# Performance work log

Measured on AMD Instinct MI355X. Metric: run time of the kernel, lower is better.

## Reference

```python
import jax, jax.numpy as jnp
import numpy as np

H, W = 224, 224
WS = 7            # window size
SHIFT = 3         # shift_size = window_size // 2
C = 256           # embed_dim
NH = 4            # num heads
HD = C // NH      # head dim
N = WS * WS       # tokens per window
B = 4
HIDDEN = 1024
EPS = 1e-12


def _rel_pos_index():
    coords = np.stack(np.meshgrid(np.arange(WS), np.arange(WS), indexing='ij'))  # (2,WS,WS)
    cf = coords.reshape(2, -1)
    rel = (cf[:, :, None] - cf[:, None, :]).transpose(1, 2, 0)  # (N,N,2)
    rel[:, :, 0] += WS - 1
    rel[:, :, 1] += WS - 1
    rel[:, :, 0] *= 2 * WS - 1
    return rel.sum(-1)  # (N,N) int

REL_IDX = _rel_pos_index()


def _shift_mask():
    img = np.zeros((H, W))
    cnt = 0
    for hs in (slice(0, -WS), slice(-WS, -SHIFT), slice(-SHIFT, None)):
        for ws_ in (slice(0, -WS), slice(-WS, -SHIFT), slice(-SHIFT, None)):
            img[hs, ws_] = cnt
            cnt += 1
    mw = img.reshape(H // WS, WS, W // WS, WS).transpose(0, 2, 1, 3).reshape(-1, N)
    am = mw[:, None, :] - mw[:, :, None]  # (nW, N, N)
    return np.where(am != 0, -100.0, 0.0).astype(np.float32)

SHIFT_MASK = _shift_mask()  # (nW, N, N)


def layer_norm(x, g, b):
    mu = x.mean(-1, keepdims=True)
    var = ((x - mu) ** 2).mean(-1, keepdims=True)
    return (x - mu) / jnp.sqrt(var + EPS) * g + b


def partition(x, shift):
    x = x.reshape(B, H, W, C)
    if shift > 0:
        x = jnp.roll(x, (-shift, -shift), axis=(1, 2))
    x = x.reshape(B, H // WS, WS, W // WS, WS, C).transpose(0, 1, 3, 2, 4, 5)
    return x.reshape(-1, N, C)  # (B*nW, N, C)


def reverse(x, shift):
    x = x.reshape(B, H // WS, W // WS, WS, WS, C).transpose(0, 1, 3, 2, 4, 5).reshape(B, H, W, C)
    if shift > 0:
        x = jnp.roll(x, (shift, shift), axis=(1, 2))
    return x.reshape(B, H * W, C)


def window_attn(q, k, v, wq, bq, wk, bk, wv, bv, wp, bp, rpb, bool_mask, shift_mask):
    B_ = q.shape[0]
    scale = HD ** -0.5
    qh = (q @ wq + bq).reshape(B_, N, NH, HD).transpose(0, 2, 1, 3) * scale
    kh = (k @ wk + bk).reshape(B_, N, NH, HD).transpose(0, 2, 1, 3)
    vh = (v @ wv + bv).reshape(B_, N, NH, HD).transpose(0, 2, 1, 3)
    attn = jnp.einsum('bhnd,bhmd->bhnm', qh, kh)  # (B_, NH, N, N)
    attn = jnp.where(bool_mask, -1e9, attn)       # masked_fill_(attn_mask, -1e9)
    bias = rpb[REL_IDX.reshape(-1)].reshape(N, N, NH).transpose(2, 0, 1)  # (NH,N,N)
    attn = attn + bias[None]
    if shift_mask is not None:
        nW = shift_mask.shape[0]
        attn = attn.reshape(B_ // nW, nW, NH, N, N) + shift_mask[None, :, None]
        attn = attn.reshape(B_, NH, N, N)
    attn = jax.nn.softmax(attn, axis=-1)
    out = jnp.einsum('bhnm,bhmd->bhnd', attn, vh).transpose(0, 2, 1, 3).reshape(B_, N, C)
    return out @ wp + bp


def _forward(mask_dec_inputs, enc_outputs, dec_enc_attn_mask,
             ln1_g, ln1_b, ln2_g, ln2_b, ln3_g, ln3_b,
             wq1, bq1, wk1, bk1, wv1, bv1, wp1, bp1, rpb1,
             wq2, bq2, wk2, bk2, wv2, bv2, wp2, bp2, rpb2,
             fc1_w, fc1_b, fc2_w, fc2_b):
    sm = jnp.asarray(SHIFT_MASK)
    # --- block 1: plain windowed cross-attention ---
    shortcut1 = mask_dec_inputs
    y = layer_norm(mask_dec_inputs, ln1_g, ln1_b)
    enc_w = partition(enc_outputs, 0)
    y_w = partition(y, 0)
    a1 = window_attn(y_w, enc_w, enc_w, wq1, bq1, wk1, bk1, wv1, bv1, wp1, bp1,
                     rpb1, dec_enc_attn_mask, None)
    x = shortcut1 + reverse(a1, 0)
    enc = reverse(enc_w, 0)  # identity round-trip, matches original
    # --- block 2: shifted windowed cross-attention with shift mask ---
    shortcut2 = x
    y = layer_norm(x, ln2_g, ln2_b)
    enc_s = partition(enc, SHIFT)
    y_s = partition(y, SHIFT)
    a2 = window_attn(y_s, enc_s, enc_s, wq2, bq2, wk2, bk2, wv2, bv2, wp2, bp2,
                     rpb2, dec_enc_attn_mask, sm)
    x = shortcut2 + reverse(a2, SHIFT)
    # --- MLP ---
    y = layer_norm(x, ln3_g, ln3_b)
    h = jax.nn.gelu(y @ fc1_w + fc1_b, approximate=False)
    x = x + (h @ fc2_w + fc2_b)
    return x


def setup_inputs() -> dict:
    key = jax.random.key(0)
    ks = jax.random.split(key, 16)
    d = {}
    d['mask_dec_inputs'] = jax.random.normal(ks[0], (B, H * W, C), dtype=jnp.float32)
    d['enc_outputs'] = jax.random.normal(ks[1], (B, H * W, C), dtype=jnp.float32)
    d['self_attn_mask'] = jnp.zeros((1,), dtype=bool)
    d['dec_enc_attn_mask'] = jnp.zeros((1, 1, N, N), dtype=bool)
    d['ln1_g'] = jnp.ones((C,)); d['ln1_b'] = jnp.zeros((C,))
    d['ln2_g'] = jnp.ones((C,)); d['ln2_b'] = jnp.zeros((C,))
    d['ln3_g'] = jnp.ones((C,)); d['ln3_b'] = jnp.zeros((C,))
    s = 0.02
    for i, p in enumerate(['1', '2']):
        kk = jax.random.split(ks[2 + i], 5)
        d['wq' + p] = jax.random.normal(kk[0], (C, C)) * s
        d['wk' + p] = jax.random.normal(kk[1], (C, C)) * s
        d['wv' + p] = jax.random.normal(kk[2], (C, C)) * s
        d['wp' + p] = jax.random.normal(kk[3], (C, C)) * s
        d['bq' + p] = jnp.zeros((C,)); d['bk' + p] = jnp.zeros((C,))
        d['bv' + p] = jnp.zeros((C,)); d['bp' + p] = jnp.zeros((C,))
        d['rpb' + p] = jax.random.normal(kk[4], ((2 * WS - 1) ** 2, NH)) * s
    d['fc1_w'] = jax.random.normal(ks[4], (C, HIDDEN)) * s
    d['fc1_b'] = jnp.zeros((HIDDEN,))
    d['fc2_w'] = jax.random.normal(ks[5], (HIDDEN, C)) * s
    d['fc2_b'] = jnp.zeros((C,))
    return d


def reference(mask_dec_inputs, enc_outputs, self_attn_mask, dec_enc_attn_mask,
              ln1_g, ln1_b, ln2_g, ln2_b, ln3_g, ln3_b,
              wq1, bq1, wk1, bk1, wv1, bv1, wp1, bp1, rpb1,
              wq2, bq2, wk2, bk2, wv2, bv2, wp2, bp2, rpb2,
              fc1_w, fc1_b, fc2_w, fc2_b):
    # self_attn_mask is accepted but unused, matching the original forward
    return _forward(mask_dec_inputs, enc_outputs, dec_enc_attn_mask,
                    ln1_g, ln1_b, ln2_g, ln2_b, ln3_g, ln3_b,
                    wq1, bq1, wk1, bk1, wv1, bv1, wp1, bp1, rpb1,
                    wq2, bq2, wk2, bk2, wv2, bv2, wp2, bp2, rpb2,
                    fc1_w, fc1_b, fc2_w, fc2_b)
```

## Files before the change

### kernel.cpp

```cpp
#include <hip/hip_runtime.h>

typedef unsigned short u16;
typedef __bf16 bf16x8 __attribute__((ext_vector_type(8)));
typedef float f32x4 __attribute__((ext_vector_type(4)));

#define T_TOK 200704
#define NTOK 49
#define SA 264
#define SP 72

__device__ __forceinline__ u16 f2bf(float f) {
    union { float f; unsigned u; } v; v.f = f;
    return (u16)((v.u + 0x7FFFu + ((v.u >> 16) & 1u)) >> 16);
}
__device__ __forceinline__ bf16x8 zfrag() {
    bf16x8 z;
#pragma unroll
    for (int i = 0; i < 8; ++i) z[i] = (__bf16)0.0f;
    return z;
}

__global__ void k_transpose(const float* __restrict__ in, u16* __restrict__ out, int K, int N) {
    int idx = blockIdx.x * blockDim.x + threadIdx.x;
    if (idx >= K * N) return;
    int k = idx / N, n = idx - k * N;
    out[n * K + k] = f2bf(in[idx]);
}

__device__ __forceinline__ void gemm49h(const u16* A, const u16* WT,
                                        int nb, int mtb, int lane, f32x4 acc[2][4]) {
    const int ar = lane & 15;
    const int kg = (lane >> 4) * 8;
    const bf16x8 z = zfrag();
    for (int k0 = 0; k0 < 256; k0 += 32) {
        bf16x8 a[2], bb[4];
#pragma unroll
        for (int m = 0; m < 2; ++m) {
            int row = (mtb + m) * 16 + ar;
            a[m] = (row < NTOK) ? *(const bf16x8*)(A + row * SA + k0 + kg) : z;
        }
#pragma unroll
        for (int nt = 0; nt < 4; ++nt) {
            int col = nb + nt * 16 + ar;
            bb[nt] = *(const bf16x8*)(WT + col * 256 + k0 + kg);
        }
#pragma unroll
        for (int m = 0; m < 2; ++m)
#pragma unroll
            for (int nt = 0; nt < 4; ++nt)
                acc[m][nt] = __builtin_amdgcn_mfma_f32_16x16x32_bf16(a[m], bb[nt], acc[m][nt], 0, 0, 0);
    }
}

__global__ __launch_bounds__(512, 4) void k_win_attn(
    const float* src, float* dst, const float* __restrict__ enc,
    const float* __restrict__ lng, const float* __restrict__ lnb,
    const u16* __restrict__ wqT, const u16* __restrict__ wkT,
    const u16* __restrict__ wvT, const u16* __restrict__ wpT,
    const float* __restrict__ bq, const float* __restrict__ bk,
    const float* __restrict__ bv, const float* __restrict__ bp,
    const float* __restrict__ rpb, int shift)
{
    __shared__ __align__(16) char smem[80384];
    u16* tA = (u16*)(smem);
    u16* tB = (u16*)(smem + 25872);
    u16* tC = (u16*)(smem + 54096);
    int* t_idx = (int*)(smem + 79968);
    int* label = (int*)(smem + 80164);

    const int tid = threadIdx.x, lane = tid & 63;
    const int w = tid >> 6;
    const int s  = w & 3;
    const int hf = w >> 2;
    const int mtb = hf * 2;
    const int l15 = lane & 15, g = lane >> 4, kg = g * 8;
    const int nb = s * 64;

    const int wi = blockIdx.x;
    const int b  = wi >> 10;
    const int wl = wi & 1023;
    const int wh = wl >> 5, wwi = wl & 31;

    if (tid < NTOK) {
        int yi = tid / 7, xi = tid - yi * 7;
        int h = wh * 7 + yi + shift; if (h >= 224) h -= 224;
        int ww = wwi * 7 + xi + shift; if (ww >= 224) ww -= 224;
        t_idx[tid] = (b * 224 + h) * 224 + ww;
        int hp = wh * 7 + yi, wp = wwi * 7 + xi;
        int rh = (hp < 217) ? 0 : ((hp < 221) ? 1 : 2);
        int rw = (wp < 217) ? 0 : ((wp < 221) ? 1 : 2);
        label[tid] = rh * 3 + rw;
    }
    __syncthreads();

    for (int r = w; r < NTOK; r += 8) {
        const float4 xv = *(const float4*)(src + (size_t)t_idx[r] * 256 + lane * 4);
        float xs[4] = {xv.x, xv.y, xv.z, xv.w};
        float sm = xs[0] + xs[1] + xs[2] + xs[3];
        float s2 = xs[0] * xs[0] + xs[1] * xs[1] + xs[2] * xs[2] + xs[3] * xs[3];
#pragma unroll
        for (int m = 1; m < 64; m <<= 1) { sm += __shfl_xor(sm, m); s2 += __shfl_xor(s2, m); }
        float mean = sm * (1.0f / 256.0f);
        float var = s2 * (1.0f / 256.0f) - mean * mean;
        float rstd = rsqrtf(fmaxf(var, 0.0f) + 1e-12f);
#pragma unroll
        for (int j = 0; j < 4; ++j) {
            int c = lane * 4 + j;
            float yv = (xs[j] - mean) * rstd * lng[c] + lnb[c];
            tA[r * SA + c] = f2bf(yv);
        }
    }
    __syncthreads();

    {
        f32x4 acc[2][4] = {};
        gemm49h(tA, wqT, nb, mtb, lane, acc);
#pragma unroll
        for (int m = 0; m < 2; ++m)
#pragma unroll
            for (int nt = 0; nt < 4; ++nt) {
                int col = nb + nt * 16 + l15;
                float bias = bq[col];
#pragma unroll
                for (int r = 0; r < 4; ++r) {
                    int row = (mtb + m) * 16 + g * 4 + r;
                    if (row < NTOK) tB[row * SA + col] = f2bf((acc[m][nt][r] + bias) * 0.125f);
                }
            }
    }
    __syncthreads();

    for (int idx = tid; idx < NTOK * 32; idx += 512) {
        int r = idx >> 5, c8 = (idx & 31) << 3;
        const float* ep = enc + (size_t)t_idx[r] * 256 + c8;
        const float4 v0 = *(const float4*)(ep);
        const float4 v1 = *(const float4*)(ep + 4);
        u16* p = tA + r * SA + c8;
        p[0] = f2bf(v0.x); p[1] = f2bf(v0.y); p[2] = f2bf(v0.z); p[3] = f2bf(v0.w);
        p[4] = f2bf(v1.x); p[5] = f2bf(v1.y); p[6] = f2bf(v1.z); p[7] = f2bf(v1.w);
    }
    __syncthreads();

    {
        f32x4 acc[2][4] = {};
        gemm49h(tA, wkT, nb, mtb, lane, acc);
#pragma unroll
        for (int m = 0; m < 2; ++m)
#pragma unroll
            for (int nt = 0; nt < 4; ++nt) {
                int col = nb + nt * 16 + l15;
                float bias = bk[col];
#pragma unroll
                for (int r = 0; r < 4; ++r) {
                    int row = (mtb + m) * 16 + g * 4 + r;
                    if (row < NTOK) tC[row * SA + col] = f2bf(acc[m][nt][r] + bias);
                }
            }
    }
    __syncthreads();

    f32x4 vacc[2][4] = {};
    gemm49h(tA, wvT, nb, mtb, lane, vacc);

    f32x4 sa[2][4] = {};
    {
        const int h = s;
        const bf16x8 z = zfrag();
        for (int k0 = 0; k0 < 64; k0 += 32) {
            bf16x8 a[2], bb[4];
#pragma unroll
            for (int m = 0; m < 2; ++m) {
                int row = (mtb + m) * 16 + l15;
                a[m] = (row < NTOK) ? *(const bf16x8*)(tB + row * SA + h * 64 + k0 + kg) : z;
            }
#pragma unroll
            for (int nt = 0; nt < 4; ++nt) {
                int col = nt * 16 + l15;
                bb[nt] = (col < NTOK) ? *(const bf16x8*)(tC + col * SA + h * 64 + k0 + kg) : z;
            }
#pragma unroll
            for (int m = 0; m < 2; ++m)
#pragma unroll
                for (int nt = 0; nt < 4; ++nt)
                    sa[m][nt] = __builtin_amdgcn_mfma_f32_16x16x32_bf16(a[m], bb[nt], sa[m][nt], 0, 0, 0);
        }
#pragma unroll
        for (int m = 0; m < 2; ++m) {
#pragma unroll
            for (int rr = 0; rr < 4; ++rr) {
                int i = (mtb + m) * 16 + g * 4 + rr;
                bool iv = (i < NTOK);
                int yi = iv ? (i / 7) : 0, xi = iv ? (i - (i / 7) * 7) : 0;
                int li = iv ? label[i] : 0;
                float v[4], mx = -1e30f;
#pragma unroll
                for (int nt = 0; nt < 4; ++nt) {
                    int j = nt * 16 + l15;
                    float t = -1e30f;
                    if (iv && j < NTOK) {
                        t = sa[m][nt][rr];
                        int yj = j / 7, xj = j - (j / 7) * 7;
                        t += rpb[((yi - yj + 6) * 13 + (xi - xj + 6)) * 4 + h];
                        if (shift > 0 && li != label[j]) t -= 100.0f;
                    }
                    v[nt] = t;
                    mx = fmaxf(mx, t);
                }
#pragma unroll
                for (int mk = 1; mk < 16; mk <<= 1) mx = fmaxf(mx, __shfl_xor(mx, mk));
                float sum = 0.f, e[4];
#pragma unroll
                for (int nt = 0; nt < 4; ++nt) {
                    e[nt] = (v[nt] > -1e29f) ? __expf(v[nt] - mx) : 0.0f;
                    sum += e[nt];
                }
#pragma unroll
                for (int mk = 1; mk < 16; mk <<= 1) sum += __shfl_xor(sum, mk);
                float inv = 1.0f / sum;
#pragma unroll
                for (int nt = 0; nt < 4; ++nt) sa[m][nt][rr] = e[nt] * inv;
            }
        }
    }
    __syncthreads();

    {
        const int h = s;
#pragma unroll
        for (int m = 0; m < 2; ++m)
#pragma unroll
            for (int rr = 0; rr < 4; ++rr) {
                int i = (mtb + m) * 16 + g * 4 + rr;
                if (i < NTOK) {
                    u16* Prow = tB + h * (NTOK * SP) + i * SP;
#pragma unroll
                    for (int nt = 0; nt < 4; ++nt) Prow[nt * 16 + l15] = f2bf(sa[m][nt][rr]);
                }
            }
#pragma unroll
        for (int m = 0; m < 2; ++m)
#pragma unroll
            for (int nt = 0; nt < 4; ++nt) {
                int col = nb + nt * 16 + l15;
                float bias = bv[col];
#pragma unroll
                for (int r = 0; r < 4; ++r) {
                    int row = (mtb + m) * 16 + g * 4 + r;
                    if (row < NTOK) tC[row * SA + col] = f2bf(vacc[m][nt][r] + bias);
                }
            }
    }
    __syncthreads();

    {
        const int h = s;
        const bf16x8 z = zfrag();
        f32x4 oa[2][4] = {};
        for (int k0 = 0; k0 < 64; k0 += 32) {
            bf16x8 a[2], bb[4];
#pragma unroll
            for (int m = 0; m < 2; ++m) {
                int row = (mtb + m) * 16 + l15;
                a[m] = (row < NTOK) ? *(const bf16x8*)(tB + h * (NTOK * SP) + row * SP + k0 + kg) : z;
            }
#pragma unroll
            for (int nt = 0; nt < 4; ++nt) {
                u16 tmp[8];
#pragma unroll
                for (int i = 0; i < 8; ++i) {
                    int tok = k0 + kg + i;
                    tmp[i] = (tok < NTOK) ? tC[tok * SA + h * 64 + nt * 16 + l15] : (u16)0;
                }
                bb[nt] = *(bf16x8*)tmp;
            }
#pragma unroll
            for (int m = 0; m < 2; ++m)
#pragma unroll
                for (int nt = 0; nt < 4; ++nt)
                    oa[m][nt] = __builtin_amdgcn_mfma_f32_16x16x32_bf16(a[m], bb[nt], oa[m][nt], 0, 0, 0);
        }
#pragma unroll
        for (int m = 0; m < 2; ++m)
#pragma unroll
            for (int nt = 0; nt < 4; ++nt) {
                int col = h * 64 + nt * 16 + l15;
#pragma unroll
                for (int r = 0; r < 4; ++r) {
                    int row = (mtb + m) * 16 + g * 4 + r;
                    if (row < NTOK) tA[row * SA + col] = f2bf(oa[m][nt][r]);
                }
            }
    }
    __syncthreads();

    {
        f32x4 acc[2][4] = {};
        gemm49h(tA, wpT, nb, mtb, lane, acc);
#pragma unroll
        for (int m = 0; m < 2; ++m)
#pragma unroll
            for (int nt = 0; nt < 4; ++nt) {
                int col = nb + nt * 16 + l15;
                float bias = bp[col];
#pragma unroll
                for (int r = 0; r < 4; ++r) {
                    int row = (mtb + m) * 16 + g * 4 + r;
                    if (row < NTOK) {
                        size_t off = (size_t)t_idx[row] * 256 + col;
                        dst[off] = src[off] + acc[m][nt][r] + bias;
                    }
                }
            }
    }
}

#define SM 264
__global__ __launch_bounds__(256) void k_mlp(
    float* R,
    const float* __restrict__ lng, const float* __restrict__ lnb,
    const u16* __restrict__ fc1T, const float* __restrict__ fc1b,
    const u16* __restrict__ fc2T, const float* __restrict__ fc2b)
{
    __shared__ __align__(16) u16 yL[64 * SM];
    __shared__ __align__(16) u16 hL[64 * SM];
    const int tid = threadIdx.x, lane = tid & 63, wave = tid >> 6;
    const size_t t0 = (size_t)blockIdx.x * 64;

    for (int r = wave; r < 64; r += 4) {
        const float4 xv = *(const float4*)(R + (t0 + r) * 256 + lane * 4);
        float xs[4] = {xv.x, xv.y, xv.z, xv.w};
        float s = xs[0] + xs[1] + xs[2] + xs[3];
        float s2 = xs[0] * xs[0] + xs[1] * xs[1] + xs[2] * xs[2] + xs[3] * xs[3];
#pragma unroll
        for (int m = 1; m < 64; m <<= 1) { s += __shfl_xor(s, m); s2 += __shfl_xor(s2, m); }
        float mean = s * (1.0f / 256.0f);
        float var = s2 * (1.0f / 256.0f) - mean * mean;
        float rstd = rsqrtf(fmaxf(var, 0.0f) + 1e-12f);
#pragma unroll
        for (int j = 0; j < 4; ++j) {
            int c = lane * 4 + j;
            float yv = (xs[j] - mean) * rstd * lng[c] + lnb[c];
            yL[r * SM + c] = f2bf(yv);
        }
    }
    __syncthreads();

    const int nb = wave * 64;
    const int ar = lane & 15;
    const int kg = (lane >> 4) * 8;
    f32x4 acc2[4][4] = {};
    for (int ch = 0; ch < 4; ++ch) {
        f32x4 acc1[4][4] = {};
        for (int k0 = 0; k0 < 256; k0 += 32) {
            bf16x8 a[4], bb[4];
#pragma unroll
            for (int mt = 0; mt < 4; ++mt)
                a[mt] = *(const bf16x8*)(yL + (mt * 16 + ar) * SM + k0 + kg);
#pragma unroll
            for (int nt = 0; nt < 4; ++nt) {
                int hidx = ch * 256 + nb + nt * 16 + ar;
                bb[nt] = *(const bf16x8*)(fc1T + (size_t)hidx * 256 + k0 + kg);
            }
#pragma unroll
            for (int mt = 0; mt < 4; ++mt)
#pragma unroll
                for (int nt = 0; nt < 4; ++nt)
                    acc1[mt][nt] = __builtin_amdgcn_mfma_f32_16x16x32_bf16(a[mt], bb[nt], acc1[mt][nt], 0, 0, 0);
        }
#pragma unroll
        for (int mt = 0; mt < 4; ++mt)
#pragma unroll
            for (int nt = 0; nt < 4; ++nt) {
                int lcol = nb + nt * 16 + (lane & 15);
                float bias = fc1b[ch * 256 + lcol];
#pragma unroll
                for (int r = 0; r < 4; ++r) {
                    int row = mt * 16 + (lane >> 4) * 4 + r;
                    float v = acc1[mt][nt][r] + bias;
                    v = 0.5f * v * (1.0f + erff(v * 0.70710678f));
                    hL[row * SM + lcol] = f2bf(v);
                }
            }
        __syncthreads();
        for (int k0 = 0; k0 < 256; k0 += 32) {
            bf16x8 a[4], bb[4];
#pragma unroll
            for (int mt = 0; mt < 4; ++mt)
                a[mt] = *(const bf16x8*)(hL + (mt * 16 + ar) * SM + k0 + kg);
#pragma unroll
            for (int nt = 0; nt < 4; ++nt) {
                int col = nb + nt * 16 + ar;
                bb[nt] = *(const bf16x8*)(fc2T + (size_t)col * 1024 + ch * 256 + k0 + kg);
            }
#pragma unroll
            for (int mt = 0; mt < 4; ++mt)
#pragma unroll
                for (int nt = 0; nt < 4; ++nt)
                    acc2[mt][nt] = __builtin_amdgcn_mfma_f32_16x16x32_bf16(a[mt], bb[nt], acc2[mt][nt], 0, 0, 0);
        }
        __syncthreads();
    }
#pragma unroll
    for (int mt = 0; mt < 4; ++mt)
#pragma unroll
        for (int nt = 0; nt < 4; ++nt) {
            int col = nb + nt * 16 + (lane & 15);
            float bias = fc2b[col];
#pragma unroll
            for (int r = 0; r < 4; ++r) {
                int row = mt * 16 + (lane >> 4) * 4 + r;
                size_t off = (t0 + row) * 256 + col;
                R[off] = acc2[mt][nt][r] + bias + R[off];
            }
        }
}

extern "C" void kernel_launch(void* const* d_in, const int* in_sizes, int n_in,
                              void* d_out, int out_size, void* d_ws, size_t ws_size,
                              hipStream_t stream) {
    (void)in_sizes; (void)n_in; (void)out_size; (void)ws_size;
    u16* WTbase = (u16*)d_ws;
    u16* wT[8];
    for (int i = 0; i < 8; ++i) wT[i] = WTbase + (size_t)i * 65536;
    u16* fc1T = WTbase + (size_t)8 * 65536;
    u16* fc2T = fc1T + 262144;

    const int wsrc[8] = {10, 11, 12, 13, 19, 20, 21, 22};
    for (int i = 0; i < 8; ++i)
        k_transpose<<<256, 256, 0, stream>>>((const float*)d_in[wsrc[i]], wT[i], 256, 256);
    k_transpose<<<1024, 256, 0, stream>>>((const float*)d_in[28], fc1T, 256, 1024);
    k_transpose<<<1024, 256, 0, stream>>>((const float*)d_in[30], fc2T, 1024, 256);

    float* R = (float*)d_out;

    k_win_attn<<<4096, 512, 0, stream>>>((const float*)d_in[0], R, (const float*)d_in[1],
        (const float*)d_in[4], (const float*)d_in[5],
        wT[0], wT[1], wT[2], wT[3],
        (const float*)d_in[14], (const float*)d_in[15], (const float*)d_in[16], (const float*)d_in[17],
        (const float*)d_in[18], 0);
    k_win_attn<<<4096, 512, 0, stream>>>(R, R, (const float*)d_in[1],
        (const float*)d_in[6], (const float*)d_in[7],
        wT[4], wT[5], wT[6], wT[7],
        (const float*)d_in[23], (const float*)d_in[24], (const float*)d_in[25], (const float*)d_in[26],
        (const float*)d_in[27], 3);
    k_mlp<<<T_TOK / 64, 256, 0, stream>>>(R,
        (const float*)d_in[8], (const float*)d_in[9],
        fc1T, (const float*)d_in[29], fc2T, (const float*)d_in[31]);
}
```

Measured before the change: 2.065 ms.

## Precompute K/V projections of encoder output once, gather per window in attention

```diff
diff --git a/kernel.cpp b/kernel.cpp
--- a/kernel.cpp
+++ b/kernel.cpp
@@ -52,7 +52,283 @@
     }
 }
 
-__global__ __launch_bounds__(512, 4) void k_win_attn(
+__global__ __launch_bounds__(256, 4) void k_kv(
+    const float* __restrict__ enc, u16* __restrict__ KV,
+    const u16* __restrict__ w0T, const u16* __restrict__ w1T,
+    const u16* __restrict__ w2T, const u16* __restrict__ w3T,
+    const float* __restrict__ b0, const float* __restrict__ b1,
+    const float* __restrict__ b2, const float* __restrict__ b3)
+{
+    __shared__ __align__(16) u16 aL[64 * SA];
+    const int tid = threadIdx.x, lane = tid & 63, w = tid >> 6;
+    const int gy = blockIdx.y;
+    const u16* WT = (gy == 0) ? w0T : (gy == 1) ? w1T : (gy == 2) ? w2T : w3T;
+    const float* bs = (gy == 0) ? b0 : (gy == 1) ? b1 : (gy == 2) ? b2 : b3;
+    const size_t t0 = (size_t)blockIdx.x * 64;
+
+    for (int idx = tid; idx < 64 * 32; idx += 256) {
+        int r = idx >> 5, c8 = (idx & 31) << 3;
+        const float* ep = enc + (t0 + r) * 256 + c8;
+        const float4 v0 = *(const float4*)ep;
+        const float4 v1 = *(const float4*)(ep + 4);
+        u16* p = aL + r * SA + c8;
+        p[0] = f2bf(v0.x); p[1] = f2bf(v0.y); p[2] = f2bf(v0.z); p[3] = f2bf(v0.w);
+        p[4] = f2bf(v1.x); p[5] = f2bf(v1.y); p[6] = f2bf(v1.z); p[7] = f2bf(v1.w);
+    }
+    __syncthreads();
+
+    const int nb = w * 64, ar = lane & 15, g = lane >> 4, kg = g * 8;
+    f32x4 acc[4][4] = {};
+    for (int k0 = 0; k0 < 256; k0 += 32) {
+        bf16x8 a[4], bb[4];
+#pragma unroll
+        for (int mt = 0; mt < 4; ++mt)
+            a[mt] = *(const bf16x8*)(aL + (mt * 16 + ar) * SA + k0 + kg);
+#pragma unroll
+        for (int nt = 0; nt < 4; ++nt)
+            bb[nt] = *(const bf16x8*)(WT + (nb + nt * 16 + ar) * 256 + k0 + kg);
+#pragma unroll
+        for (int mt = 0; mt < 4; ++mt)
+#pragma unroll
+            for (int nt = 0; nt < 4; ++nt)
+                acc[mt][nt] = __builtin_amdgcn_mfma_f32_16x16x32_bf16(a[mt], bb[nt], acc[mt][nt], 0, 0, 0);
+    }
+#pragma unroll
+    for (int mt = 0; mt < 4; ++mt)
+#pragma unroll
+        for (int nt = 0; nt < 4; ++nt) {
+            int col = nb + nt * 16 + (lane & 15);
+            float bias = bs[col];
+#pragma unroll
+            for (int r = 0; r < 4; ++r) {
+                int row = mt * 16 + g * 4 + r;
+                KV[(t0 + row) * 1024 + gy * 256 + col] = f2bf(acc[mt][nt][r] + bias);
+            }
+        }
+}
+
+__global__ __launch_bounds__(512, 4) void k_win_attn2(
+    const float* src, float* dst, const u16* __restrict__ KV, int kvoff,
+    const float* __restrict__ lng, const float* __restrict__ lnb,
+    const u16* __restrict__ wqT, const u16* __restrict__ wpT,
+    const float* __restrict__ bq, const float* __restrict__ bp,
+    const float* __restrict__ rpb, int shift)
+{
+    __shared__ __align__(16) char smem[80384];
+    u16* tA = (u16*)(smem);
+    u16* tB = (u16*)(smem + 25872);
+    u16* tC = (u16*)(smem + 54096);
+    int* t_idx = (int*)(smem + 79968);
+    int* label = (int*)(smem + 80164);
+
+    const int tid = threadIdx.x, lane = tid & 63;
+    const int w = tid >> 6;
+    const int s  = w & 3;
+    const int hf = w >> 2;
+    const int mtb = hf * 2;
+    const int l15 = lane & 15, g = lane >> 4, kg = g * 8;
+    const int nb = s * 64;
+
+    const int wi = blockIdx.x;
+    const int b  = wi >> 10;
+    const int wl = wi & 1023;
+    const int wh = wl >> 5, wwi = wl & 31;
+
+    if (tid < NTOK) {
+        int yi = tid / 7, xi = tid - yi * 7;
+        int h = wh * 7 + yi + shift; if (h >= 224) h -= 224;
+        int ww = wwi * 7 + xi + shift; if (ww >= 224) ww -= 224;
+        t_idx[tid] = (b * 224 + h) * 224 + ww;
+        int hp = wh * 7 + yi, wp = wwi * 7 + xi;
+        int rh = (hp < 217) ? 0 : ((hp < 221) ? 1 : 2);
+        int rw = (wp < 217) ? 0 : ((wp < 221) ? 1 : 2);
+        label[tid] = rh * 3 + rw;
+    }
+    __syncthreads();
+
+    if (hf == 0) {
+        for (int r = s; r < NTOK; r += 4) {
+            const float4 xv = *(const float4*)(src + (size_t)t_idx[r] * 256 + lane * 4);
+            float xs[4] = {xv.x, xv.y, xv.z, xv.w};
+            float sm = xs[0] + xs[1] + xs[2] + xs[3];
+            float s2 = xs[0] * xs[0] + xs[1] * xs[1] + xs[2] * xs[2] + xs[3] * xs[3];
+#pragma unroll
+            for (int m = 1; m < 64; m <<= 1) { sm += __shfl_xor(sm, m); s2 += __shfl_xor(s2, m); }
+            float mean = sm * (1.0f / 256.0f);
+            float var = s2 * (1.0f / 256.0f) - mean * mean;
+            float rstd = rsqrtf(fmaxf(var, 0.0f) + 1e-12f);
+#pragma unroll
+            for (int j = 0; j < 4; ++j) {
+                int c = lane * 4 + j;
+                float yv = (xs[j] - mean) * rstd * lng[c] + lnb[c];
+                tA[r * SA + c] = f2bf(yv);
+            }
+        }
+    } else {
+        for (int r = s; r < NTOK; r += 4)
+            *(ushort4*)(tC + r * SA + lane * 4) =
+                *(const ushort4*)(KV + (size_t)t_idx[r] * 1024 + kvoff + lane * 4);
+    }
+    __syncthreads();
+
+    {
+        f32x4 acc[2][4] = {};
+        gemm49h(tA, wqT, nb, mtb, lane, acc);
+#pragma unroll
+        for (int m = 0; m < 2; ++m)
+#pragma unroll
+            for (int nt = 0; nt < 4; ++nt) {
+                int col = nb + nt * 16 + l15;
+                float bias = bq[col];
+#pragma unroll
+                for (int r = 0; r < 4; ++r) {
+                    int row = (mtb + m) * 16 + g * 4 + r;
+                    if (row < NTOK) tB[row * SA + col] = f2bf((acc[m][nt][r] + bias) * 0.125f);
+                }
+            }
+    }
+    __syncthreads();
+
+    for (int r = w; r < NTOK; r += 8)
+        *(ushort4*)(tA + r * SA + lane * 4) =
+            *(const ushort4*)(KV + (size_t)t_idx[r] * 1024 + kvoff + 256 + lane * 4);
+
+    f32x4 sa[2][4] = {};
+    {
+        const int h = s;
+        const bf16x8 z = zfrag();
+        for (int k0 = 0; k0 < 64; k0 += 32) {
+            bf16x8 a[2], bb[4];
+#pragma unroll
+            for (int m = 0; m < 2; ++m) {
+                int row = (mtb + m) * 16 + l15;
+                a[m] = (row < NTOK) ? *(const bf16x8*)(tB + row * SA + h * 64 + k0 + kg) : z;
+            }
+#pragma unroll
+            for (int nt = 0; nt < 4; ++nt) {
+                int col = nt * 16 + l15;
+                bb[nt] = (col < NTOK) ? *(const bf16x8*)(tC + col * SA + h * 64 + k0 + kg) : z;
+            }
+#pragma unroll
+            for (int m = 0; m < 2; ++m)
+#pragma unroll
+                for (int nt = 0; nt < 4; ++nt)
+                    sa[m][nt] = __builtin_amdgcn_mfma_f32_16x16x32_bf16(a[m], bb[nt], sa[m][nt], 0, 0, 0);
+        }
+#pragma unroll
+        for (int m = 0; m < 2; ++m) {
+#pragma unroll
+            for (int rr = 0; rr < 4; ++rr) {
+                int i = (mtb + m) * 16 + g * 4 + rr;
+                bool iv = (i < NTOK);
+                int yi = iv ? (i / 7) : 0, xi = iv ? (i - (i / 7) * 7) : 0;
+                int li = iv ? label[i] : 0;
+                float v[4], mx = -1e30f;
+#pragma unroll
+                for (int nt = 0; nt < 4; ++nt) {
+                    int j = nt * 16 + l15;
+                    float t = -1e30f;
+                    if (iv && j < NTOK) {
+                        t = sa[m][nt][rr];
+                        int yj = j / 7, xj = j - (j / 7) * 7;
+                        t += rpb[((yi - yj + 6) * 13 + (xi - xj + 6)) * 4 + h];
+                        if (shift > 0 && li != label[j]) t -= 100.0f;
+                    }
+                    v[nt] = t;
+                    mx = fmaxf(mx, t);
+                }
+#pragma unroll
+                for (int mk = 1; mk < 16; mk <<= 1) mx = fmaxf(mx, __shfl_xor(mx, mk));
+                float sum = 0.f, e[4];
+#pragma unroll
+                for (int nt = 0; nt < 4; ++nt) {
+                    e[nt] = (v[nt] > -1e29f) ? __expf(v[nt] - mx) : 0.0f;
+                    sum += e[nt];
+                }
+#pragma unroll
+                for (int mk = 1; mk < 16; mk <<= 1) sum += __shfl_xor(sum, mk);
+                float inv = 1.0f / sum;
+#pragma unroll
+                for (int nt = 0; nt < 4; ++nt) sa[m][nt][rr] = e[nt] * inv;
+            }
+        }
+    }
+    __syncthreads();
+
+    {
+        const int h = s;
+#pragma unroll
+        for (int m = 0; m < 2; ++m)
+#pragma unroll
+            for (int rr = 0; rr < 4; ++rr) {
+                int i = (mtb + m) * 16 + g * 4 + rr;
+                if (i < NTOK) {
+                    u16* Prow = tB + h * (NTOK * SP) + i * SP;
+#pragma unroll
+                    for (int nt = 0; nt < 4; ++nt) Prow[nt * 16 + l15] = f2bf(sa[m][nt][rr]);
+                }
+            }
+        const bf16x8 z = zfrag();
+        f32x4 oa[2][4] = {};
+        for (int k0 = 0; k0 < 64; k0 += 32) {
+            bf16x8 a[2], bb[4];
+#pragma unroll
+            for (int m = 0; m < 2; ++m) {
+                int row = (mtb + m) * 16 + l15;
+                a[m] = (row < NTOK) ? *(const bf16x8*)(tB + h * (NTOK * SP) + row * SP + k0 + kg) : z;
+            }
+#pragma unroll
+            for (int nt = 0; nt < 4; ++nt) {
+                u16 tmp[8];
+#pragma unroll
+                for (int i = 0; i < 8; ++i) {
+                    int tok = k0 + kg + i;
+                    tmp[i] = (tok < NTOK) ? tA[tok * SA + h * 64 + nt * 16 + l15] : (u16)0;
+                }
+                bb[nt] = *(bf16x8*)tmp;
+            }
+#pragma unroll
+            for (int m = 0; m < 2; ++m)
+#pragma unroll
+                for (int nt = 0; nt < 4; ++nt)
+                    oa[m][nt] = __builtin_amdgcn_mfma_f32_16x16x32_bf16(a[m], bb[nt], oa[m][nt], 0, 0, 0);
+        }
+#pragma unroll
+        for (int m = 0; m < 2; ++m)
+#pragma unroll
+            for (int nt = 0; nt < 4; ++nt) {
+                int col = h * 64 + nt * 16 + l15;
+#pragma unroll
+                for (int r = 0; r < 4; ++r) {
+                    int row = (mtb + m) * 16 + g * 4 + r;
+                    if (row < NTOK) tC[row * SA + col] = f2bf(oa[m][nt][r]);
+                }
+            }
+    }
+    __syncthreads();
+
+    {
+        f32x4 acc[2][4] = {};
+        gemm49h(tC, wpT, nb, mtb, lane, acc);
+#pragma unroll
+        for (int m = 0; m < 2; ++m)
+#pragma unroll
+            for (int nt = 0; nt < 4; ++nt) {
+                int col = nb + nt * 16 + l15;
+                float bias = bp[col];
+#pragma unroll
+                for (int r = 0; r < 4; ++r) {
+                    int row = (mtb + m) * 16 + g * 4 + r;
+                    if (row < NTOK) {
+                        size_t off = (size_t)t_idx[row] * 256 + col;
+                        dst[off] = src[off] + acc[m][nt][r] + bias;
+                    }
+                }
+            }
+    }
+}
+
+__global__ __launch_bounds__(512, 4) void k_win_attn_fb(
     const float* src, float* dst, const float* __restrict__ enc,
     const float* __restrict__ lng, const float* __restrict__ lnb,
     const u16* __restrict__ wqT, const u16* __restrict__ wkT,
@@ -106,8 +382,7 @@
 #pragma unroll
         for (int j = 0; j < 4; ++j) {
             int c = lane * 4 + j;
-            float yv = (xs[j] - mean) * rstd * lng[c] + lnb[c];
-            tA[r * SA + c] = f2bf(yv);
+            tA[r * SA + c] = f2bf((xs[j] - mean) * rstd * lng[c] + lnb[c]);
         }
     }
     __syncthreads();
@@ -279,6 +554,7 @@
                 for (int nt = 0; nt < 4; ++nt)
                     oa[m][nt] = __builtin_amdgcn_mfma_f32_16x16x32_bf16(a[m], bb[nt], oa[m][nt], 0, 0, 0);
         }
+        __syncthreads();
 #pragma unroll
         for (int m = 0; m < 2; ++m)
 #pragma unroll
@@ -315,7 +591,7 @@
 }
 
 #define SM 264
-__global__ __launch_bounds__(256) void k_mlp(
+__global__ __launch_bounds__(512, 4) void k_mlp(
     float* R,
     const float* __restrict__ lng, const float* __restrict__ lnb,
     const u16* __restrict__ fc1T, const float* __restrict__ fc1b,
@@ -323,94 +599,93 @@
 {
     __shared__ __align__(16) u16 yL[64 * SM];
     __shared__ __align__(16) u16 hL[64 * SM];
-    const int tid = threadIdx.x, lane = tid & 63, wave = tid >> 6;
+    const int tid = threadIdx.x, lane = tid & 63, w = tid >> 6;
+    const int s2 = w & 3, hf = w >> 2, mtb = hf * 2;
+    const int l15 = lane & 15, g = lane >> 4, kg = g * 8;
     const size_t t0 = (size_t)blockIdx.x * 64;
-
-    for (int r = wave; r < 64; r += 4) {
+    const int nb = s2 * 64;
+
+    for (int r = w; r < 64; r += 8) {
         const float4 xv = *(const float4*)(R + (t0 + r) * 256 + lane * 4);
         float xs[4] = {xv.x, xv.y, xv.z, xv.w};
         float s = xs[0] + xs[1] + xs[2] + xs[3];
-        float s2 = xs[0] * xs[0] + xs[1] * xs[1] + xs[2] * xs[2] + xs[3] * xs[3];
-#pragma unroll
-        for (int m = 1; m < 64; m <<= 1) { s += __shfl_xor(s, m); s2 += __shfl_xor(s2, m); }
+        float s2s = xs[0] * xs[0] + xs[1] * xs[1] + xs[2] * xs[2] + xs[3] * xs[3];
+#pragma unroll
+        for (int m = 1; m < 64; m <<= 1) { s += __shfl_xor(s, m); s2s += __shfl_xor(s2s, m); }
         float mean = s * (1.0f / 256.0f);
-        float var = s2 * (1.0f / 256.0f) - mean * mean;
+        float var = s2s * (1.0f / 256.0f) - mean * mean;
         float rstd = rsqrtf(fmaxf(var, 0.0f) + 1e-12f);
 #pragma unroll
         for (int j = 0; j < 4; ++j) {
             int c = lane * 4 + j;
-            float yv = (xs[j] - mean) * rstd * lng[c] + lnb[c];
-            yL[r * SM + c] = f2bf(yv);
-        }
-    }
-    __syncthreads();
-
-    const int nb = wave * 64;
-    const int ar = lane & 15;
-    const int kg = (lane >> 4) * 8;
-    f32x4 acc2[4][4] = {};
+            yL[r * SM + c] = f2bf((xs[j] - mean) * rstd * lng[c] + lnb[c]);
+        }
+    }
+    __syncthreads();
+
+    f32x4 acc2[2][4] = {};
     for (int ch = 0; ch < 4; ++ch) {
-        f32x4 acc1[4][4] = {};
+        f32x4 acc1[2][4] = {};
         for (int k0 = 0; k0 < 256; k0 += 32) {
-            bf16x8 a[4], bb[4];
-#pragma unroll
-            for (int mt = 0; mt < 4; ++mt)
-                a[mt] = *(const bf16x8*)(yL + (mt * 16 + ar) * SM + k0 + kg);
-#pragma unroll
-            for (int nt = 0; nt < 4; ++nt) {
-                int hidx = ch * 256 + nb + nt * 16 + ar;
+            bf16x8 a[2], bb[4];
+#pragma unroll
+            for (int m = 0; m < 2; ++m)
+                a[m] = *(const bf16x8*)(yL + ((mtb + m) * 16 + l15) * SM + k0 + kg);
+#pragma unroll
+            for (int nt = 0; nt < 4; ++nt) {
+                int hidx = ch * 256 + nb + nt * 16 + l15;
                 bb[nt] = *(const bf16x8*)(fc1T + (size_t)hidx * 256 + k0 + kg);
             }
 #pragma unroll
-            for (int mt = 0; mt < 4; ++mt)
+            for (int m = 0; m < 2; ++m)
 #pragma unroll
                 for (int nt = 0; nt < 4; ++nt)
-                    acc1[mt][nt] = __builtin_amdgcn_mfma_f32_16x16x32_bf16(a[mt], bb[nt], acc1[mt][nt], 0, 0, 0);
-        }
-#pragma unroll
-        for (int mt = 0; mt < 4; ++mt)
-#pragma unroll
-            for (int nt = 0; nt < 4; ++nt) {
-                int lcol = nb + nt * 16 + (lane & 15);
-                float bias = fc1b[ch * 256 + lcol];
-#pragma unroll
-                for (int r = 0; r < 4; ++r) {
-                    int row = mt * 16 + (lane >> 4) * 4 + r;
-                    float v = acc1[mt][nt][r] + bias;
+                    acc1[m][nt] = __builtin_amdgcn_mfma_f32_16x16x32_bf16(a[m], bb[nt], acc1[m][nt], 0, 0, 0);
+        }
+#pragma unroll
+        for (int m = 0; m < 2; ++m)
+#pragma unroll
+            for (int nt = 0; nt < 4; ++nt) {
+                int hcol = nb + nt * 16 + l15;
+                float bias = fc1b[ch * 256 + hcol];
+#pragma unroll
+                for (int r = 0; r < 4; ++r) {
+                    int row = (mtb + m) * 16 + g * 4 + r;
+                    float v = acc1[m][nt][r] + bias;
                     v = 0.5f * v * (1.0f + erff(v * 0.70710678f));
-                    hL[row * SM + lcol] = f2bf(v);
+                    hL[row * SM + hcol] = f2bf(v);
                 }
             }
         __syncthreads();
         for (int k0 = 0; k0 < 256; k0 += 32) {
-            bf16x8 a[4], bb[4];
-#pragma unroll
-            for (int mt = 0; mt < 4; ++mt)
-                a[mt] = *(const bf16x8*)(hL + (mt * 16 + ar) * SM + k0 + kg);
-#pragma unroll
-            for (int nt = 0; nt < 4; ++nt) {
-                int col = nb + nt * 16 + ar;
+            bf16x8 a[2], bb[4];
+#pragma unroll
+            for (int m = 0; m < 2; ++m)
+                a[m] = *(const bf16x8*)(hL + ((mtb + m) * 16 + l15) * SM + k0 + kg);
+#pragma unroll
+            for (int nt = 0; nt < 4; ++nt) {
+                int col = nb + nt * 16 + l15;
                 bb[nt] = *(const bf16x8*)(fc2T + (size_t)col * 1024 + ch * 256 + k0 + kg);
             }
 #pragma unroll
-            for (int mt = 0; mt < 4; ++mt)
+            for (int m = 0; m < 2; ++m)
 #pragma unroll
                 for (int nt = 0; nt < 4; ++nt)
-                    acc2[mt][nt] = __builtin_amdgcn_mfma_f32_16x16x32_bf16(a[mt], bb[nt], acc2[mt][nt], 0, 0, 0);
+                    acc2[m][nt] = __builtin_amdgcn_mfma_f32_16x16x32_bf16(a[m], bb[nt], acc2[m][nt], 0, 0, 0);
         }
         __syncthreads();
     }
 #pragma unroll
-    for (int mt = 0; mt < 4; ++mt)
+    for (int m = 0; m < 2; ++m)
 #pragma unroll
         for (int nt = 0; nt < 4; ++nt) {
-            int col = nb + nt * 16 + (lane & 15);
+            int col = nb + nt * 16 + l15;
             float bias = fc2b[col];
 #pragma unroll
             for (int r = 0; r < 4; ++r) {
-                int row = mt * 16 + (lane >> 4) * 4 + r;
+                int row = (mtb + m) * 16 + g * 4 + r;
                 size_t off = (t0 + row) * 256 + col;
-                R[off] = acc2[mt][nt][r] + bias + R[off];
+                R[off] = acc2[m][nt][r] + bias + R[off];
             }
         }
 }
@@ -418,12 +693,15 @@
 extern "C" void kernel_launch(void* const* d_in, const int* in_sizes, int n_in,
                               void* d_out, int out_size, void* d_ws, size_t ws_size,
                               hipStream_t stream) {
-    (void)in_sizes; (void)n_in; (void)out_size; (void)ws_size;
+    (void)in_sizes; (void)n_in; (void)out_size;
     u16* WTbase = (u16*)d_ws;
     u16* wT[8];
     for (int i = 0; i < 8; ++i) wT[i] = WTbase + (size_t)i * 65536;
     u16* fc1T = WTbase + (size_t)8 * 65536;
     u16* fc2T = fc1T + 262144;
+    u16* KV = WTbase + 1048576;
+    const size_t need = 2u * 1024 * 1024 + (size_t)T_TOK * 1024 * 2;
+    const bool big = (ws_size >= need);
 
     const int wsrc[8] = {10, 11, 12, 13, 19, 20, 21, 22};
     for (int i = 0; i < 8; ++i)
@@ -433,17 +711,31 @@
 
     float* R = (float*)d_out;
 
-    k_win_attn<<<4096, 512, 0, stream>>>((const float*)d_in[0], R, (const float*)d_in[1],
-        (const float*)d_in[4], (const float*)d_in[5],
-        wT[0], wT[1], wT[2], wT[3],
-        (const float*)d_in[14], (const float*)d_in[15], (const float*)d_in[16], (const float*)d_in[17],
-        (const float*)d_in[18], 0);
-    k_win_attn<<<4096, 512, 0, stream>>>(R, R, (const float*)d_in[1],
-        (const float*)d_in[6], (const float*)d_in[7],
-        wT[4], wT[5], wT[6], wT[7],
-        (const float*)d_in[23], (const float*)d_in[24], (const float*)d_in[25], (const float*)d_in[26],
-        (const float*)d_in[27], 3);
-    k_mlp<<<T_TOK / 64, 256, 0, stream>>>(R,
+    if (big) {
+        dim3 gkv(T_TOK / 64, 4);
+        k_kv<<<gkv, 256, 0, stream>>>((const float*)d_in[1], KV,
+            wT[1], wT[2], wT[5], wT[6],
+            (const float*)d_in[15], (const float*)d_in[16],
+            (const float*)d_in[24], (const float*)d_in[25]);
+        k_win_attn2<<<4096, 512, 0, stream>>>((const float*)d_in[0], R, KV, 0,
+            (const float*)d_in[4], (const float*)d_in[5], wT[0], wT[3],
+            (const float*)d_in[14], (const float*)d_in[17], (const float*)d_in[18], 0);
+        k_win_attn2<<<4096, 512, 0, stream>>>(R, R, KV, 512,
+            (const float*)d_in[6], (const float*)d_in[7], wT[4], wT[7],
+            (const float*)d_in[23], (const float*)d_in[26], (const float*)d_in[27], 3);
+    } else {
+        k_win_attn_fb<<<4096, 512, 0, stream>>>((const float*)d_in[0], R, (const float*)d_in[1],
+            (const float*)d_in[4], (const float*)d_in[5],
+            wT[0], wT[1], wT[2], wT[3],
+            (const float*)d_in[14], (const float*)d_in[15], (const float*)d_in[16], (const float*)d_in[17],
+            (const float*)d_in[18], 0);
+        k_win_attn_fb<<<4096, 512, 0, stream>>>(R, R, (const float*)d_in[1],
+            (const float*)d_in[6], (const float*)d_in[7],
+            wT[4], wT[5], wT[6], wT[7],
+            (const float*)d_in[23], (const float*)d_in[24], (const float*)d_in[25], (const float*)d_in[26],
+            (const float*)d_in[27], 3);
+    }
+    k_mlp<<<T_TOK / 64, 512, 0, stream>>>(R,
         (const float*)d_in[8], (const float*)d_in[9],
         fc1T, (const float*)d_in[29], fc2T, (const float*)d_in[31]);
 }
```

New measurement: 2.262 ms. +9.5%, slower.

## Precompute K/V projections of encoder output in a separate token-parallel GEMM kernel

Applied to the files above, without the earlier changes.

```diff
diff --git a/kernel.cpp b/kernel.cpp
--- a/kernel.cpp
+++ b/kernel.cpp
@@ -52,13 +52,68 @@
     }
 }
 
-__global__ __launch_bounds__(512, 4) void k_win_attn(
-    const float* src, float* dst, const float* __restrict__ enc,
+__global__ __launch_bounds__(256, 4) void k_kv(
+    const float* __restrict__ enc, u16* __restrict__ KV,
+    const u16* __restrict__ w0T, const u16* __restrict__ w1T,
+    const u16* __restrict__ w2T, const u16* __restrict__ w3T,
+    const float* __restrict__ b0, const float* __restrict__ b1,
+    const float* __restrict__ b2, const float* __restrict__ b3)
+{
+    __shared__ __align__(16) u16 aL[64 * SA];
+    const int tid = threadIdx.x, lane = tid & 63, w = tid >> 6;
+    const size_t t0 = (size_t)blockIdx.x * 64;
+    const int nb = w * 64, ar = lane & 15, g = lane >> 4, kg = g * 8;
+
+    for (int idx = tid; idx < 64 * 32; idx += 256) {
+        int r = idx >> 5, c8 = (idx & 31) << 3;
+        const float* ep = enc + (t0 + r) * 256 + c8;
+        const float4 v0 = *(const float4*)ep;
+        const float4 v1 = *(const float4*)(ep + 4);
+        u16* p = aL + r * SA + c8;
+        p[0] = f2bf(v0.x); p[1] = f2bf(v0.y); p[2] = f2bf(v0.z); p[3] = f2bf(v0.w);
+        p[4] = f2bf(v1.x); p[5] = f2bf(v1.y); p[6] = f2bf(v1.z); p[7] = f2bf(v1.w);
+    }
+    __syncthreads();
+
+    const u16* Ws[4] = {w0T, w1T, w2T, w3T};
+    const float* Bs[4] = {b0, b1, b2, b3};
+#pragma unroll
+    for (int t = 0; t < 4; ++t) {
+        f32x4 acc[4][4] = {};
+        for (int k0 = 0; k0 < 256; k0 += 32) {
+            bf16x8 a[4], bb[4];
+#pragma unroll
+            for (int mt = 0; mt < 4; ++mt)
+                a[mt] = *(const bf16x8*)(aL + (mt * 16 + ar) * SA + k0 + kg);
+#pragma unroll
+            for (int nt = 0; nt < 4; ++nt)
+                bb[nt] = *(const bf16x8*)(Ws[t] + (nb + nt * 16 + ar) * 256 + k0 + kg);
+#pragma unroll
+            for (int mt = 0; mt < 4; ++mt)
+#pragma unroll
+                for (int nt = 0; nt < 4; ++nt)
+                    acc[mt][nt] = __builtin_amdgcn_mfma_f32_16x16x32_bf16(a[mt], bb[nt], acc[mt][nt], 0, 0, 0);
+        }
+#pragma unroll
+        for (int mt = 0; mt < 4; ++mt)
+#pragma unroll
+            for (int nt = 0; nt < 4; ++nt) {
+                int col = nb + nt * 16 + (lane & 15);
+                float bias = Bs[t][col];
+#pragma unroll
+                for (int r = 0; r < 4; ++r) {
+                    int row = mt * 16 + g * 4 + r;
+                    KV[(t0 + row) * 1024 + t * 256 + col] = f2bf(acc[mt][nt][r] + bias);
+                }
+            }
+    }
+}
+
+__global__ __launch_bounds__(512, 4) void k_win_attn2(
+    const float* src, float* dst, const u16* __restrict__ KV, int kvoff,
     const float* __restrict__ lng, const float* __restrict__ lnb,
-    const u16* __restrict__ wqT, const u16* __restrict__ wkT,
-    const u16* __restrict__ wvT, const u16* __restrict__ wpT,
-    const float* __restrict__ bq, const float* __restrict__ bk,
-    const float* __restrict__ bv, const float* __restrict__ bp,
+    const u16* __restrict__ wqT, const u16* __restrict__ wpT,
+    const float* __restrict__ bq, const float* __restrict__ bp,
     const float* __restrict__ rpb, int shift)
 {
     __shared__ __align__(16) char smem[80384];
@@ -93,22 +148,27 @@
     }
     __syncthreads();
 
-    for (int r = w; r < NTOK; r += 8) {
-        const float4 xv = *(const float4*)(src + (size_t)t_idx[r] * 256 + lane * 4);
-        float xs[4] = {xv.x, xv.y, xv.z, xv.w};
-        float sm = xs[0] + xs[1] + xs[2] + xs[3];
-        float s2 = xs[0] * xs[0] + xs[1] * xs[1] + xs[2] * xs[2] + xs[3] * xs[3];
-#pragma unroll
-        for (int m = 1; m < 64; m <<= 1) { sm += __shfl_xor(sm, m); s2 += __shfl_xor(s2, m); }
-        float mean = sm * (1.0f / 256.0f);
-        float var = s2 * (1.0f / 256.0f) - mean * mean;
-        float rstd = rsqrtf(fmaxf(var, 0.0f) + 1e-12f);
-#pragma unroll
-        for (int j = 0; j < 4; ++j) {
-            int c = lane * 4 + j;
-            float yv = (xs[j] - mean) * rstd * lng[c] + lnb[c];
-            tA[r * SA + c] = f2bf(yv);
-        }
+    if (hf == 0) {
+        for (int r = s; r < NTOK; r += 4) {
+            const float4 xv = *(const float4*)(src + (size_t)t_idx[r] * 256 + lane * 4);
+            float xs[4] = {xv.x, xv.y, xv.z, xv.w};
+            float sm = xs[0] + xs[1] + xs[2] + xs[3];
+            float s2 = xs[0] * xs[0] + xs[1] * xs[1] + xs[2] * xs[2] + xs[3] * xs[3];
+#pragma unroll
+            for (int m = 1; m < 64; m <<= 1) { sm += __shfl_xor(sm, m); s2 += __shfl_xor(s2, m); }
+            float mean = sm * (1.0f / 256.0f);
+            float var = s2 * (1.0f / 256.0f) - mean * mean;
+            float rstd = rsqrtf(fmaxf(var, 0.0f) + 1e-12f);
+#pragma unroll
+            for (int j = 0; j < 4; ++j) {
+                int c = lane * 4 + j;
+                tA[r * SA + c] = f2bf((xs[j] - mean) * rstd * lng[c] + lnb[c]);
+            }
+        }
+    } else {
+        for (int r = s; r < NTOK; r += 4)
+            *(ushort4*)(tC + r * SA + lane * 4) =
+                *(const ushort4*)(KV + (size_t)t_idx[r] * 1024 + kvoff + lane * 4);
     }
     __syncthreads();
 
@@ -124,59 +184,32 @@
 #pragma unroll
                 for (int r = 0; r < 4; ++r) {
                     int row = (mtb + m) * 16 + g * 4 + r;
-                    if (row < NTOK) tB[row * SA + col] = f2bf((acc[m][nt][r] + bias) * 0.125f);
-                }
-            }
-    }
-    __syncthreads();
-
-    for (int idx = tid; idx < NTOK * 32; idx += 512) {
-        int r = idx >> 5, c8 = (idx & 31) << 3;
-        const float* ep = enc + (size_t)t_idx[r] * 256 + c8;
-        const float4 v0 = *(const float4*)(ep);
-        const float4 v1 = *(const float4*)(ep + 4);
-        u16* p = tA + r * SA + c8;
-        p[0] = f2bf(v0.x); p[1] = f2bf(v0.y); p[2] = f2bf(v0.z); p[3] = f2bf(v0.w);
-        p[4] = f2bf(v1.x); p[5] = f2bf(v1.y); p[6] = f2bf(v1.z); p[7] = f2bf(v1.w);
-    }
-    __syncthreads();
-
-    {
-        f32x4 acc[2][4] = {};
-        gemm49h(tA, wkT, nb, mtb, lane, acc);
-#pragma unroll
-        for (int m = 0; m < 2; ++m)
-#pragma unroll
-            for (int nt = 0; nt < 4; ++nt) {
-                int col = nb + nt * 16 + l15;
-                float bias = bk[col];
-#pragma unroll
-                for (int r = 0; r < 4; ++r) {
-                    int row = (mtb + m) * 16 + g * 4 + r;
-                    if (row < NTOK) tC[row * SA + col] = f2bf(acc[m][nt][r] + bias);
-                }
-            }
-    }
-    __syncthreads();
-
-    f32x4 vacc[2][4] = {};
-    gemm49h(tA, wvT, nb, mtb, lane, vacc);
+                    if (row < NTOK)
+                        tB[s * (NTOK * SP) + row * SP + nt * 16 + l15] =
+                            f2bf((acc[m][nt][r] + bias) * 0.125f);
+                }
+            }
+    }
+    __syncthreads();
+
+    for (int r = w; r < NTOK; r += 8)
+        *(ushort4*)(tA + r * SA + lane * 4) =
+            *(const ushort4*)(KV + (size_t)t_idx[r] * 1024 + kvoff + 256 + lane * 4);
 
     f32x4 sa[2][4] = {};
     {
-        const int h = s;
         const bf16x8 z = zfrag();
         for (int k0 = 0; k0 < 64; k0 += 32) {
             bf16x8 a[2], bb[4];
 #pragma unroll
             for (int m = 0; m < 2; ++m) {
                 int row = (mtb + m) * 16 + l15;
-                a[m] = (row < NTOK) ? *(const bf16x8*)(tB + row * SA + h * 64 + k0 + kg) : z;
+                a[m] = (row < NTOK) ? *(const bf16x8*)(tB + s * (NTOK * SP) + row * SP + k0 + kg) : z;
             }
 #pragma unroll
             for (int nt = 0; nt < 4; ++nt) {
                 int col = nt * 16 + l15;
-                bb[nt] = (col < NTOK) ? *(const bf16x8*)(tC + col * SA + h * 64 + k0 + kg) : z;
+                bb[nt] = (col < NTOK) ? *(const bf16x8*)(tC + col * SA + s * 64 + k0 + kg) : z;
             }
 #pragma unroll
             for (int m = 0; m < 2; ++m)
@@ -200,7 +233,7 @@
                     if (iv && j < NTOK) {
                         t = sa[m][nt][rr];
                         int yj = j / 7, xj = j - (j / 7) * 7;
-                        t += rpb[((yi - yj + 6) * 13 + (xi - xj + 6)) * 4 + h];
+                        t += rpb[((yi - yj + 6) * 13 + (xi - xj + 6)) * 4 + s];
                         if (shift > 0 && li != label[j]) t -= 100.0f;
                     }
                     v[nt] = t;
@@ -224,44 +257,26 @@
     }
     __syncthreads();
 
+    f32x4 oa[2][4] = {};
     {
-        const int h = s;
 #pragma unroll
         for (int m = 0; m < 2; ++m)
 #pragma unroll
             for (int rr = 0; rr < 4; ++rr) {
                 int i = (mtb + m) * 16 + g * 4 + rr;
                 if (i < NTOK) {
-                    u16* Prow = tB + h * (NTOK * SP) + i * SP;
+                    u16* Prow = tB + s * (NTOK * SP) + i * SP;
 #pragma unroll
                     for (int nt = 0; nt < 4; ++nt) Prow[nt * 16 + l15] = f2bf(sa[m][nt][rr]);
                 }
             }
-#pragma unroll
-        for (int m = 0; m < 2; ++m)
-#pragma unroll
-            for (int nt = 0; nt < 4; ++nt) {
-                int col = nb + nt * 16 + l15;
-                float bias = bv[col];
-#pragma unroll
-                for (int r = 0; r < 4; ++r) {
-                    int row = (mtb + m) * 16 + g * 4 + r;
-                    if (row < NTOK) tC[row * SA + col] = f2bf(vacc[m][nt][r] + bias);
-                }
-            }
-    }
-    __syncthreads();
-
-    {
-        const int h = s;
         const bf16x8 z = zfrag();
-        f32x4 oa[2][4] = {};
         for (int k0 = 0; k0 < 64; k0 += 32) {
             bf16x8 a[2], bb[4];
 #pragma unroll
             for (int m = 0; m < 2; ++m) {
                 int row = (mtb + m) * 16 + l15;
-                a[m] = (row < NTOK) ? *(const bf16x8*)(tB + h * (NTOK * SP) + row * SP + k0 + kg) : z;
+                a[m] = (row < NTOK) ? *(const bf16x8*)(tB + s * (NTOK * SP) + row * SP + k0 + kg) : z;
             }
 #pragma unroll
             for (int nt = 0; nt < 4; ++nt) {
@@ -269,7 +284,7 @@
 #pragma unroll
                 for (int i = 0; i < 8; ++i) {
                     int tok = k0 + kg + i;
-                    tmp[i] = (tok < NTOK) ? tC[tok * SA + h * 64 + nt * 16 + l15] : (u16)0;
+                    tmp[i] = (tok < NTOK) ? tA[tok * SA + s * 64 + nt * 16 + l15] : (u16)0;
                 }
                 bb[nt] = *(bf16x8*)tmp;
             }
@@ -279,23 +294,24 @@
                 for (int nt = 0; nt < 4; ++nt)
                     oa[m][nt] = __builtin_amdgcn_mfma_f32_16x16x32_bf16(a[m], bb[nt], oa[m][nt], 0, 0, 0);
         }
-#pragma unroll
-        for (int m = 0; m < 2; ++m)
-#pragma unroll
-            for (int nt = 0; nt < 4; ++nt) {
-                int col = h * 64 + nt * 16 + l15;
-#pragma unroll
-                for (int r = 0; r < 4; ++r) {
-                    int row = (mtb + m) * 16 + g * 4 + r;
-                    if (row < NTOK) tA[row * SA + col] = f2bf(oa[m][nt][r]);
-                }
-            }
-    }
+    }
+    __syncthreads();
+#pragma unroll
+    for (int m = 0; m < 2; ++m)
+#pragma unroll
+        for (int nt = 0; nt < 4; ++nt) {
+            int col = s * 64 + nt * 16 + l15;
+#pragma unroll
+            for (int r = 0; r < 4; ++r) {
+                int row = (mtb + m) * 16 + g * 4 + r;
+                if (row < NTOK) tB[row * SA + col] = f2bf(oa[m][nt][r]);
+            }
+        }
     __syncthreads();
 
     {
         f32x4 acc[2][4] = {};
-        gemm49h(tA, wpT, nb, mtb, lane, acc);
+        gemm49h(tB, wpT, nb, mtb, lane, acc);
 #pragma unroll
         for (int m = 0; m < 2; ++m)
 #pragma unroll
@@ -339,8 +355,7 @@
 #pragma unroll
         for (int j = 0; j < 4; ++j) {
             int c = lane * 4 + j;
-            float yv = (xs[j] - mean) * rstd * lng[c] + lnb[c];
-            yL[r * SM + c] = f2bf(yv);
+            yL[r * SM + c] = f2bf((xs[j] - mean) * rstd * lng[c] + lnb[c]);
         }
     }
     __syncthreads();
@@ -424,6 +439,7 @@
     for (int i = 0; i < 8; ++i) wT[i] = WTbase + (size_t)i * 65536;
     u16* fc1T = WTbase + (size_t)8 * 65536;
     u16* fc2T = fc1T + 262144;
+    u16* KV = WTbase + 1048576;
 
     const int wsrc[8] = {10, 11, 12, 13, 19, 20, 21, 22};
     for (int i = 0; i < 8; ++i)
@@ -433,16 +449,16 @@
 
     float* R = (float*)d_out;
 
-    k_win_attn<<<4096, 512, 0, stream>>>((const float*)d_in[0], R, (const float*)d_in[1],
-        (const float*)d_in[4], (const float*)d_in[5],
-        wT[0], wT[1], wT[2], wT[3],
-        (const float*)d_in[14], (const float*)d_in[15], (const float*)d_in[16], (const float*)d_in[17],
-        (const float*)d_in[18], 0);
-    k_win_attn<<<4096, 512, 0, stream>>>(R, R, (const float*)d_in[1],
-        (const float*)d_in[6], (const float*)d_in[7],
-        wT[4], wT[5], wT[6], wT[7],
-        (const float*)d_in[23], (const float*)d_in[24], (const float*)d_in[25], (const float*)d_in[26],
-        (const float*)d_in[27], 3);
+    k_kv<<<T_TOK / 64, 256, 0, stream>>>((const float*)d_in[1], KV,
+        wT[1], wT[2], wT[5], wT[6],
+        (const float*)d_in[15], (const float*)d_in[16],
+        (const float*)d_in[24], (const float*)d_in[25]);
+    k_win_attn2<<<4096, 512, 0, stream>>>((const float*)d_in[0], R, KV, 0,
+        (const float*)d_in[4], (const float*)d_in[5], wT[0], wT[3],
+        (const float*)d_in[14], (const float*)d_in[17], (const float*)d_in[18], 0);
+    k_win_attn2<<<4096, 512, 0, stream>>>(R, R, KV, 512,
+        (const float*)d_in[6], (const float*)d_in[7], wT[4], wT[7],
+        (const float*)d_in[23], (const float*)d_in[26], (const float*)d_in[27], 3);
     k_mlp<<<T_TOK / 64, 256, 0, stream>>>(R,
         (const float*)d_in[8], (const float*)d_in[9],
         fc1T, (const float*)d_in[29], fc2T, (const float*)d_in[31]);
```

Measured after the change: 2.089 ms. About the same (+1.1%).
